# Optimization experiments

Measured on AMD Instinct MI355X. Metric: run time of the kernel, lower is better.

Reference implementation:

```python
import jax, jax.numpy as jnp
import numpy as np

N = 50000
E = 800000
F_IN = 128
HID = 32
C = 16


def setup_inputs() -> dict:
    key = jax.random.key(0)
    ks = jax.random.split(key, 8)
    x = jax.random.normal(ks[0], (N, F_IN), dtype=jnp.float32)
    edge_index = jax.random.randint(ks[1], (2, E), 0, N, dtype=jnp.int64)
    edge_attr = jax.random.uniform(ks[2], (E,), dtype=jnp.float32)
    W_rel1 = jax.random.normal(ks[3], (F_IN, HID), dtype=jnp.float32) / np.sqrt(F_IN)
    W_root1 = jax.random.normal(ks[4], (F_IN, HID), dtype=jnp.float32) / np.sqrt(F_IN)
    b1 = jnp.zeros((HID,), dtype=jnp.float32)
    W_rel2 = jax.random.normal(ks[5], (HID, C), dtype=jnp.float32) / np.sqrt(HID)
    W_root2 = jax.random.normal(ks[6], (HID, C), dtype=jnp.float32) / np.sqrt(HID)
    b2 = jnp.zeros((C,), dtype=jnp.float32)
    return {"x": x, "edge_index": edge_index, "edge_attr": edge_attr,
            "W_rel1": W_rel1, "W_root1": W_root1, "b1": b1,
            "W_rel2": W_rel2, "W_root2": W_root2, "b2": b2}


def reference(x, edge_index, edge_attr, W_rel1, W_root1, b1, W_rel2, W_root2, b2):
    src = edge_index[0]  # message source (x_j)
    dst = edge_index[1]  # aggregation target

    def graph_conv(h, W_rel, W_root, b):
        # PyG GraphConv: out = lin_rel(sum_{j in N(i)} w_ij * h_j) + lin_root(h_i)
        msg = h[src] * edge_attr[:, None]                       # [E, d]
        agg = jax.ops.segment_sum(msg, dst, num_segments=h.shape[0])  # [N, d]
        return agg @ W_rel + h @ W_root + b

    h = jax.nn.relu(graph_conv(x, W_rel1, W_root1, b1))          # [N, 32]
    out = graph_conv(h, W_rel2, W_root2, b2)                     # [N, C]
    return jax.nn.log_softmax(out, axis=1)
```

## Files before the change

kernel.cpp:

```cpp
#include <hip/hip_runtime.h>
#include <math.h>

#define N_NODES 50000
#define E_EDGES 800000
#define F_INDIM 128
#define HID 32
#define C_OUT 16

#define BSH 7
#define BNODE 128
#define NB 391
#define BCAP 2560
#define CH 3125

#define K1ROWS 64
#define K1PAD 72
#define K1BLKS 782

typedef unsigned long long u64;
typedef unsigned short ushort_t;

__device__ __forceinline__ ushort_t bf16rne(float f) {
    unsigned u = __float_as_uint(f);
    return (ushort_t)((u + 0x7FFFu + ((u >> 16) & 1u)) >> 16);
}
__device__ __forceinline__ float bf16tof(ushort_t b) {
    return __uint_as_float((unsigned)b << 16);
}

__global__ __launch_bounds__(256) void k_init(int* __restrict__ bcur) {
    int b = blockIdx.x * 256 + threadIdx.x;
    if (b < NB) bcur[b] = b * BCAP;
}

__global__ __launch_bounds__(256) void k_fuseA(
        const float* __restrict__ x,
        const float* __restrict__ Wrel, const float* __restrict__ Wroot,
        const float* __restrict__ b1,
        const int* __restrict__ ei, const float* __restrict__ ea,
        int* __restrict__ bcur, u64* __restrict__ arena,
        ushort_t* __restrict__ t1b, float* __restrict__ t2b) {
    __shared__ __align__(16) char smem[69632];
    const int tid = threadIdx.x;

    if (blockIdx.x < 256) {
        int* hist = (int*)smem;
        int* excl = hist + 512;
        int* cur  = excl + 513;
        int* gb   = cur + NB;
        int* wsum = gb + NB;
        u64* stage = (u64*)(smem + 8192);
        const int e0 = blockIdx.x * CH;

        for (int i = tid; i < 512; i += 256) hist[i] = 0;
        __syncthreads();
        for (int k = tid; k < CH; k += 256)
            atomicAdd(&hist[ei[E_EDGES + e0 + k] >> BSH], 1);
        __syncthreads();
        {
            int v0 = hist[2 * tid], v1 = hist[2 * tid + 1];
            int s = v0 + v1, inc = s;
            int lane = tid & 63, w = tid >> 6;
#pragma unroll
            for (int d = 1; d < 64; d <<= 1) {
                int t = __shfl_up(inc, d);
                if (lane >= d) inc += t;
            }
            if (lane == 63) wsum[w] = inc;
            __syncthreads();
            int wb = 0;
            if (w > 0) wb += wsum[0];
            if (w > 1) wb += wsum[1];
            if (w > 2) wb += wsum[2];
            int ex = wb + inc - s;
            excl[2 * tid] = ex;
            excl[2 * tid + 1] = ex + v0;
        }
        __syncthreads();
        for (int b = tid; b < NB; b += 256) cur[b] = excl[b];
        __syncthreads();
        for (int k = tid; k < CH; k += 256) {
            int e = e0 + k;
            int src = ei[e];
            int dst = ei[E_EDGES + e];
            float w = ea[e];
            int bkt = dst >> BSH;
            int p = atomicAdd(&cur[bkt], 1);
            unsigned lo = (unsigned)src | ((unsigned)(dst & (BNODE - 1)) << 16)
                        | ((unsigned)bkt << 23);
            stage[p] = (u64)lo | ((u64)__float_as_uint(w) << 32);
        }
        __syncthreads();
        for (int b = tid; b < NB; b += 256) {
            int cnt = hist[b];
            gb[b] = cnt ? atomicAdd(&bcur[b], cnt) : 0;
        }
        __syncthreads();
        for (int i = tid; i < CH; i += 256) {
            u64 r = stage[i];
            int bkt = ((unsigned)r >> 23) & 0x1FF;
            arena[(size_t)gb[bkt] + (i - excl[bkt])] = r;
        }
    } else {
        float (*sW)[64] = (float(*)[64])smem;
        float (*sxT)[K1PAD] = (float(*)[K1PAD])(smem + 32768);
        const int rowBase = (blockIdx.x - 256) * K1ROWS;

        for (int i = tid; i < F_INDIM * 64; i += 256) {
            int k = i >> 6, j = i & 63;
            int c = j >> 1, m = j & 1;
            sW[k][j] = m ? Wroot[k * HID + c] : Wrel[k * HID + c];
        }
        const float4* x4 = (const float4*)x;
        for (int i = tid; i < K1ROWS * 32; i += 256) {
            int r = i >> 5, q = i & 31;
            int row = rowBase + r;
            float4 v = make_float4(0.f, 0.f, 0.f, 0.f);
            if (row < N_NODES) v = x4[(size_t)row * 32 + q];
            sxT[4 * q + 0][r] = v.x;
            sxT[4 * q + 1][r] = v.y;
            sxT[4 * q + 2][r] = v.z;
            sxT[4 * q + 3][r] = v.w;
        }
        __syncthreads();

        const int c = tid & 31;
        const int g = tid >> 5;
        float acc1[8], acc2[8];
#pragma unroll
        for (int i = 0; i < 8; ++i) { acc1[i] = 0.f; acc2[i] = 0.f; }

#pragma unroll 4
        for (int k = 0; k < F_INDIM; ++k) {
            float2 w = *(const float2*)&sW[k][2 * c];
            float4 xa = *(const float4*)&sxT[k][8 * g];
            float4 xb = *(const float4*)&sxT[k][8 * g + 4];
            acc1[0] = fmaf(xa.x, w.x, acc1[0]); acc2[0] = fmaf(xa.x, w.y, acc2[0]);
            acc1[1] = fmaf(xa.y, w.x, acc1[1]); acc2[1] = fmaf(xa.y, w.y, acc2[1]);
            acc1[2] = fmaf(xa.z, w.x, acc1[2]); acc2[2] = fmaf(xa.z, w.y, acc2[2]);
            acc1[3] = fmaf(xa.w, w.x, acc1[3]); acc2[3] = fmaf(xa.w, w.y, acc2[3]);
            acc1[4] = fmaf(xb.x, w.x, acc1[4]); acc2[4] = fmaf(xb.x, w.y, acc2[4]);
            acc1[5] = fmaf(xb.y, w.x, acc1[5]); acc2[5] = fmaf(xb.y, w.y, acc2[5]);
            acc1[6] = fmaf(xb.z, w.x, acc1[6]); acc2[6] = fmaf(xb.z, w.y, acc2[6]);
            acc1[7] = fmaf(xb.w, w.x, acc1[7]); acc2[7] = fmaf(xb.w, w.y, acc2[7]);
        }

        const float bc = b1[c];
#pragma unroll
        for (int i = 0; i < 8; ++i) {
            int row = rowBase + 8 * g + i;
            if (row < N_NODES) {
                t1b[(size_t)row * HID + c] = bf16rne(acc1[i]);
                t2b[(size_t)row * HID + c] = acc2[i] + bc;
            }
        }
    }
}

__global__ __launch_bounds__(256) void k_binB(const int* __restrict__ bcur,
                                              const u64* __restrict__ arena,
                                              unsigned* __restrict__ erec,
                                              int* __restrict__ rowptr) {
    __shared__ int hist[BNODE];
    __shared__ int excl[BNODE + 1];
    __shared__ int cur[BNODE];
    __shared__ int ws2[4];
    __shared__ int sbase;
    const int tid = threadIdx.x;
    const int b = blockIdx.x;
    if (tid < 64) {
        int acc = 0;
        for (int i = tid; i < b; i += 64) acc += bcur[i] - i * BCAP;
#pragma unroll
        for (int d = 1; d < 64; d <<= 1) acc += __shfl_xor(acc, d);
        if (tid == 0) sbase = acc;
    }
    if (tid < BNODE) hist[tid] = 0;
    __syncthreads();
    const int cnt = bcur[b] - b * BCAP;
    const u64* seg = arena + (size_t)b * BCAP;
    for (int i = tid; i < cnt; i += 256)
        atomicAdd(&hist[((unsigned)seg[i] >> 16) & (BNODE - 1)], 1);
    __syncthreads();
    {
        int v = (tid < BNODE) ? hist[tid] : 0;
        int inc = v;
        int lane = tid & 63, w = tid >> 6;
#pragma unroll
        for (int d = 1; d < 64; d <<= 1) {
            int t = __shfl_up(inc, d);
            if (lane >= d) inc += t;
        }
        if (lane == 63) ws2[w] = inc;
        __syncthreads();
        if (tid < BNODE) {
            int base = (w == 1) ? ws2[0] : 0;
            excl[tid] = base + inc - v;
        }
    }
    __syncthreads();
    const int gbase = sbase;
    if (tid < BNODE) cur[tid] = excl[tid];
    const int nodeBase = b << BSH;
    if (tid < BNODE && nodeBase + tid < N_NODES)
        rowptr[nodeBase + tid] = gbase + excl[tid];
    if (b == NB - 1 && tid == 0) rowptr[N_NODES] = E_EDGES;
    __syncthreads();
    for (int i = tid; i < cnt; i += 256) {
        u64 r = seg[i];
        unsigned lo = (unsigned)r;
        int dl = (lo >> 16) & (BNODE - 1);
        int p = atomicAdd(&cur[dl], 1);
        unsigned wu = (unsigned)(r >> 32);
        unsigned wb = (wu + 0x7FFFu + ((wu >> 16) & 1u)) & 0xFFFF0000u;
        erec[gbase + p] = wb | (lo & 0xFFFFu);
    }
}

__global__ __launch_bounds__(256) void k_gather1(
        const int* __restrict__ rowptr, const unsigned* __restrict__ erec,
        const ushort_t* __restrict__ t1b, const float* __restrict__ t2b,
        const float* __restrict__ Wrel2, const float* __restrict__ Wroot2,
        const float* __restrict__ b2,
        ushort_t* __restrict__ u1b, float* __restrict__ u2b) {
    __shared__ float sW2[HID][32];
    __shared__ float hbuf[4][HID];
    const int tid = threadIdx.x;
    const int lane = tid & 63;
    const int wid = tid >> 6;

    for (int i = tid; i < HID * 32; i += 256) {
        int k = i >> 5, j = i & 31;
        sW2[k][j] = (j >> 4) ? Wroot2[k * C_OUT + (j & 15)]
                             : Wrel2[k * C_OUT + (j & 15)];
    }

    const int node = blockIdx.x * 4 + wid;
    const int start = rowptr[node];
    const int end = rowptr[node + 1];
    const int er = lane >> 3;
    const int c4 = lane & 7;
    float ax = 0.f, ay = 0.f, az = 0.f, aw = 0.f;
    float bx = 0.f, by = 0.f, bz = 0.f, bw = 0.f;
    int e = start + er;
    for (; e + 8 < end; e += 16) {
        unsigned r0 = erec[e];
        unsigned r1 = erec[e + 8];
        float w0 = __uint_as_float(r0 & 0xFFFF0000u);
        float w1 = __uint_as_float(r1 & 0xFFFF0000u);
        ushort4 p0 = *(const ushort4*)&t1b[(size_t)(r0 & 0xFFFFu) * HID + 4 * c4];
        ushort4 p1 = *(const ushort4*)&t1b[(size_t)(r1 & 0xFFFFu) * HID + 4 * c4];
        ax = fmaf(w0, bf16tof(p0.x), ax); ay = fmaf(w0, bf16tof(p0.y), ay);
        az = fmaf(w0, bf16tof(p0.z), az); aw = fmaf(w0, bf16tof(p0.w), aw);
        bx = fmaf(w1, bf16tof(p1.x), bx); by = fmaf(w1, bf16tof(p1.y), by);
        bz = fmaf(w1, bf16tof(p1.z), bz); bw = fmaf(w1, bf16tof(p1.w), bw);
    }
    if (e < end) {
        unsigned r0 = erec[e];
        float w0 = __uint_as_float(r0 & 0xFFFF0000u);
        ushort4 p0 = *(const ushort4*)&t1b[(size_t)(r0 & 0xFFFFu) * HID + 4 * c4];
        ax = fmaf(w0, bf16tof(p0.x), ax); ay = fmaf(w0, bf16tof(p0.y), ay);
        az = fmaf(w0, bf16tof(p0.z), az); aw = fmaf(w0, bf16tof(p0.w), aw);
    }
    ax += bx; ay += by; az += bz; aw += bw;
#pragma unroll
    for (int d = 8; d < 64; d <<= 1) {
        ax += __shfl_xor(ax, d);
        ay += __shfl_xor(ay, d);
        az += __shfl_xor(az, d);
        aw += __shfl_xor(aw, d);
    }
    float4 t2 = *(const float4*)&t2b[(size_t)node * HID + 4 * c4];
    float4 hv;
    hv.x = ax + t2.x; hv.x = hv.x > 0.f ? hv.x : 0.f;
    hv.y = ay + t2.y; hv.y = hv.y > 0.f ? hv.y : 0.f;
    hv.z = az + t2.z; hv.z = hv.z > 0.f ? hv.z : 0.f;
    hv.w = aw + t2.w; hv.w = hv.w > 0.f ? hv.w : 0.f;
    if (er == 0) *(float4*)&hbuf[wid][4 * c4] = hv;
    __syncthreads();

    const int er2 = lane >> 5;
    const int j = lane & 31;
    float outv = 0.f;
#pragma unroll
    for (int kk = 0; kk < 16; ++kk) {
        int k = er2 * 16 + kk;
        outv = fmaf(hbuf[wid][k], sW2[k][j], outv);
    }
    outv += __shfl_xor(outv, 32);
    if (er2 == 0) {
        int cc = j & 15;
        if (j < 16) u1b[(size_t)node * C_OUT + cc] = bf16rne(outv);
        else        u2b[(size_t)node * C_OUT + cc] = outv + b2[cc];
    }
}

__global__ __launch_bounds__(256) void k_gather2(
        const int* __restrict__ rowptr, const unsigned* __restrict__ erec,
        const ushort_t* __restrict__ u1b, const float* __restrict__ u2b,
        float* __restrict__ out) {
    const int tid = threadIdx.x;
    const int lane = tid & 63;
    const int node = blockIdx.x * 4 + (tid >> 6);
    const int start = rowptr[node];
    const int end = rowptr[node + 1];
    const int er = lane >> 3;
    const int c2 = lane & 7;
    float a0x = 0.f, a0y = 0.f, a1x = 0.f, a1y = 0.f;
    int e = start + er;
    for (; e + 8 < end; e += 16) {
        unsigned r0 = erec[e];
        unsigned r1 = erec[e + 8];
        float w0 = __uint_as_float(r0 & 0xFFFF0000u);
        float w1 = __uint_as_float(r1 & 0xFFFF0000u);
        ushort2 p0 = *(const ushort2*)&u1b[(size_t)(r0 & 0xFFFFu) * C_OUT + 2 * c2];
        ushort2 p1 = *(const ushort2*)&u1b[(size_t)(r1 & 0xFFFFu) * C_OUT + 2 * c2];
        a0x = fmaf(w0, bf16tof(p0.x), a0x);
        a0y = fmaf(w0, bf16tof(p0.y), a0y);
        a1x = fmaf(w1, bf16tof(p1.x), a1x);
        a1y = fmaf(w1, bf16tof(p1.y), a1y);
    }
    if (e < end) {
        unsigned r0 = erec[e];
        float w0 = __uint_as_float(r0 & 0xFFFF0000u);
        ushort2 p0 = *(const ushort2*)&u1b[(size_t)(r0 & 0xFFFFu) * C_OUT + 2 * c2];
        a0x = fmaf(w0, bf16tof(p0.x), a0x);
        a0y = fmaf(w0, bf16tof(p0.y), a0y);
    }
    float ax = a0x + a1x;
    float ay = a0y + a1y;
    ax += __shfl_xor(ax, 8);  ay += __shfl_xor(ay, 8);
    ax += __shfl_xor(ax, 16); ay += __shfl_xor(ay, 16);
    ax += __shfl_xor(ax, 32); ay += __shfl_xor(ay, 32);
    float2 u2 = *(const float2*)&u2b[(size_t)node * C_OUT + 2 * c2];
    float vx = ax + u2.x;
    float vy = ay + u2.y;
    float mx = fmaxf(vx, vy);
#pragma unroll
    for (int d = 1; d < 8; d <<= 1) mx = fmaxf(mx, __shfl_xor(mx, d));
    float s = expf(vx - mx) + expf(vy - mx);
#pragma unroll
    for (int d = 1; d < 8; d <<= 1) s += __shfl_xor(s, d);
    float lse = mx + logf(s);
    if (er == 0)
        *(float2*)&out[(size_t)node * C_OUT + 2 * c2] = make_float2(vx - lse, vy - lse);
}

extern "C" void kernel_launch(void* const* d_in, const int* in_sizes, int n_in,
                              void* d_out, int out_size, void* d_ws, size_t ws_size,
                              hipStream_t stream) {
    const float* x      = (const float*)d_in[0];
    const int*   ei     = (const int*)d_in[1];
    const float* ea     = (const float*)d_in[2];
    const float* Wrel1  = (const float*)d_in[3];
    const float* Wroot1 = (const float*)d_in[4];
    const float* b1     = (const float*)d_in[5];
    const float* Wrel2  = (const float*)d_in[6];
    const float* Wroot2 = (const float*)d_in[7];
    const float* b2     = (const float*)d_in[8];
    float* out = (float*)d_out;

    float* ws = (float*)d_ws;
    float*    t2b  = ws;
    float*    u2b  = ws + 1600000;
    ushort_t* t1b  = (ushort_t*)(ws + 2400000);
    ushort_t* u1b  = (ushort_t*)(ws + 3200000);
    u64*      arena = (u64*)(ws + 3400000);
    unsigned* erec = (unsigned*)(ws + 3400000 + (size_t)NB * BCAP * 2);
    int*      bcur   = (int*)(erec + E_EDGES);
    int*      rowptr = bcur + NB;

    k_init<<<2, 256, 0, stream>>>(bcur);
    k_fuseA<<<256 + K1BLKS, 256, 0, stream>>>(
        x, Wrel1, Wroot1, b1, ei, ea, bcur, arena, t1b, t2b);
    k_binB<<<NB, 256, 0, stream>>>(bcur, arena, erec, rowptr);
    k_gather1<<<N_NODES / 4, 256, 0, stream>>>(
        rowptr, erec, t1b, t2b, Wrel2, Wroot2, b2, u1b, u2b);
    k_gather2<<<N_NODES / 4, 256, 0, stream>>>(rowptr, erec, u1b, u2b, out);
}
```

Measured before the change: 109.2 us.

## Scatter edges directly to global buckets, dropping LDS staging and prefix scan

The binning blocks used to scan their bucket histogram, stage records in shared memory in bucket order, and then copy them out to the global arena. Now each block reserves its global bucket ranges right after the histogram and writes each edge record straight to the arena at a position taken from a per-bucket shared-memory atomic counter. It also rotates the starting bucket per block to spread contention on the global atomics. This removes the scan, the staging buffer and two barriers, but the global writes become scattered rather than grouped by bucket, and the bucket id is no longer packed into the record.

```diff
diff --git a/kernel.cpp b/kernel.cpp
--- a/kernel.cpp
+++ b/kernel.cpp
@@ -45,11 +45,8 @@
 
     if (blockIdx.x < 256) {
         int* hist = (int*)smem;
-        int* excl = hist + 512;
-        int* cur  = excl + 513;
+        int* cur  = hist + 512;
         int* gb   = cur + NB;
-        int* wsum = gb + NB;
-        u64* stage = (u64*)(smem + 8192);
         const int e0 = blockIdx.x * CH;
 
         for (int i = tid; i < 512; i += 256) hist[i] = 0;
@@ -57,27 +54,12 @@
         for (int k = tid; k < CH; k += 256)
             atomicAdd(&hist[ei[E_EDGES + e0 + k] >> BSH], 1);
         __syncthreads();
-        {
-            int v0 = hist[2 * tid], v1 = hist[2 * tid + 1];
-            int s = v0 + v1, inc = s;
-            int lane = tid & 63, w = tid >> 6;
-#pragma unroll
-            for (int d = 1; d < 64; d <<= 1) {
-                int t = __shfl_up(inc, d);
-                if (lane >= d) inc += t;
-            }
-            if (lane == 63) wsum[w] = inc;
-            __syncthreads();
-            int wb = 0;
-            if (w > 0) wb += wsum[0];
-            if (w > 1) wb += wsum[1];
-            if (w > 2) wb += wsum[2];
-            int ex = wb + inc - s;
-            excl[2 * tid] = ex;
-            excl[2 * tid + 1] = ex + v0;
-        }
-        __syncthreads();
-        for (int b = tid; b < NB; b += 256) cur[b] = excl[b];
+        for (int i = tid; i < NB; i += 256) {
+            int b = i + blockIdx.x; if (b >= NB) b -= NB;
+            int cnt = hist[b];
+            gb[b] = cnt ? atomicAdd(&bcur[b], cnt) : 0;
+            cur[b] = 0;
+        }
         __syncthreads();
         for (int k = tid; k < CH; k += 256) {
             int e = e0 + k;
@@ -86,20 +68,8 @@
             float w = ea[e];
             int bkt = dst >> BSH;
             int p = atomicAdd(&cur[bkt], 1);
-            unsigned lo = (unsigned)src | ((unsigned)(dst & (BNODE - 1)) << 16)
-                        | ((unsigned)bkt << 23);
-            stage[p] = (u64)lo | ((u64)__float_as_uint(w) << 32);
-        }
-        __syncthreads();
-        for (int b = tid; b < NB; b += 256) {
-            int cnt = hist[b];
-            gb[b] = cnt ? atomicAdd(&bcur[b], cnt) : 0;
-        }
-        __syncthreads();
-        for (int i = tid; i < CH; i += 256) {
-            u64 r = stage[i];
-            int bkt = ((unsigned)r >> 23) & 0x1FF;
-            arena[(size_t)gb[bkt] + (i - excl[bkt])] = r;
+            unsigned lo = (unsigned)src | ((unsigned)(dst & (BNODE - 1)) << 16);
+            arena[(size_t)gb[bkt] + p] = (u64)lo | ((u64)__float_as_uint(w) << 32);
         }
     } else {
         float (*sW)[64] = (float(*)[64])smem;
```

Result: faster. 106.5 us (-2.5%).
